# Optimization experiments

Hardware: AMD Instinct MI355X
Metric: run time of the kernel (lower is better)

The kernel has to match this reference:

```python
import jax, jax.numpy as jnp
from jax import lax
import numpy as np

B, C, H, W = 1, 128, 32, 32
OC, K = 128, 3
STRIDE, PAD, DIL = 1, 1, 1
ARRAY_SIZE = 32
QUANT = 8


def setup_inputs() -> dict:
    key = jax.random.key(0)
    k1, k2, k3 = jax.random.split(key, 3)
    x = jax.random.normal(k1, (B, C, H, W), dtype=jnp.float32)
    weight = jax.random.normal(k2, (OC, C, K, K), dtype=jnp.float32) * 0.05
    bias = jax.random.normal(k3, (OC,), dtype=jnp.float32) * 0.05
    return {"x": x, "weight": weight, "bias": bias}


def _conv(x, w, b):
    out = lax.conv_general_dilated(
        x, w, window_strides=(STRIDE, STRIDE),
        padding=((PAD, PAD), (PAD, PAD)),
        rhs_dilation=(DIL, DIL),
        dimension_numbers=("NCHW", "OIHW", "NCHW"))
    return out + b[None, :, None, None]


def _unfold(x, oh, ow):
    # torch F.unfold: (B, C*K*K, L) with channel-major ordering (c, kh, kw)
    xp = jnp.pad(x, ((0, 0), (0, 0), (PAD, PAD), (PAD, PAD)))
    cols = jnp.stack(
        [xp[:, :, i:i + oh, j:j + ow] for i in range(K) for j in range(K)],
        axis=2)  # (B, C, K*K, OH, OW)
    return cols.reshape(B, C * K * K, oh * ow)


def reference(x, weight, bias):
    oh = (H + 2 * PAD - DIL * (K - 1) - 1) // STRIDE + 1
    ow = (W + 2 * PAD - DIL * (K - 1) - 1) // STRIDE + 1
    L = oh * ow
    qmax = float(2 ** QUANT - 1)

    # --- set_quant_params: per-spatial-location scale/zero_point from full conv out ---
    out_full = _conv(x, weight, bias).reshape(1, OC, -1)  # (1, OC, L)
    mx = jnp.max(out_full, axis=1)  # (1, L)
    mn = jnp.min(out_full, axis=1)
    scale = (mx - mn) / qmax
    zp = jnp.clip(-mn / scale, 0.0, qmax)
    zp = jnp.where(jnp.isnan(zp), 0.0, zp)
    zp = jnp.trunc(zp)  # .int() truncation
    scale = lax.stop_gradient(scale)[:, None, None, :]  # (1,1,1,L)
    zp = lax.stop_gradient(zp)[:, None, None, :]

    # --- unfold + explicit elementwise multiply (crossbar expansion) ---
    cols = _unfold(x, oh, ow)                       # (B, C*K*K, L)
    pre = cols[:, None, :, :] * weight.reshape(1, OC, C * K * K, 1)  # (B,OC,CKK,L)

    # pad front of dim 2 to a multiple of array_size (pads a full chunk if divisible)
    ckk = C * K * K
    pad_d3 = ARRAY_SIZE - ckk % ARRAY_SIZE
    pre = jnp.pad(pre, ((0, 0), (0, 0), (pad_d3, 0), (0, 0)))

    # block-sum over array_size chunks (crossbar partial sums)
    n_chunks = (ckk + pad_d3) // ARRAY_SIZE
    accu = pre.reshape(B, OC, n_chunks, ARRAY_SIZE, L).sum(axis=3)  # (B,OC,n_chunks,L)

    # per-chunk fake-quant (Quant8F) with straight-through estimator
    q = jnp.clip(jnp.round(accu / scale) + zp, 0.0, qmax)
    deq = (q - zp) * scale
    quant_accu = accu + lax.stop_gradient(deq - accu)

    # reduce over chunks -> conv output (note: bias is NOT added in original forward)
    return quant_accu.sum(axis=2).reshape(B, OC, oh, ow)
```

## Files before the change

kernel.cpp:

```cpp
#include <hip/hip_runtime.h>

#define L_    1024
#define CKK_  1152
#define QMAX_ 255.0f
#define NCH   36

__global__ __launch_bounds__(256) void wtrans(
    const float* __restrict__ w, float* __restrict__ wt)
{
    const int e  = blockIdx.x * 256 + threadIdx.x;
    const int oc = e / 288, tq = e - 288 * oc;
    const float4 v = ((const float4*)(w + oc * CKK_))[tq];
    ((float4*)wt)[tq * 128 + oc] = v;
}

template <bool WT>
__global__ __launch_bounds__(512) void fused_cas(
    const float* __restrict__ x,
    const float* __restrict__ w,
    const float4* __restrict__ wt4,
    const float* __restrict__ bias,
    float* __restrict__ out)
{
    __shared__ __align__(16) float  xs[NCH * 32 * 4];
    __shared__ __align__(16) float4 vbuf[NCH][128];
    __shared__ float red[8][4];
    __shared__ float spar[2][2][3];
    __shared__ float qb[4][128];

    const int t   = threadIdx.x;
    const int b   = blockIdx.x;
    const int oc  = t & 127;
    const int g   = t >> 7;
    const int ppe = g & 1;
    const int oh  = b >> 3;
    const int ow0 = (b & 7) * 4;
    const int l0  = b * 4;
    const int jb  = g * 9;

    const float4* wrow = (const float4*)(w + oc * CKK_);

    auto load8 = [&](float4* dst, int j) {
#pragma unroll
        for (int k4 = 0; k4 < 8; ++k4)
            dst[k4] = WT ? wt4[(j * 8 + k4) * 128 + oc] : wrow[j * 8 + k4];
    };

    float4 wA[8], wB[8], wC[8];
    load8(wA, jb + 0);
    load8(wB, jb + 1);

    for (int i = 0; i < 9; ++i) {
        const int e   = i * 512 + t;
        const int j   = e >> 7;
        const int tap = (e >> 2) & 31;
        const int px  = e & 3;
        const int d   = j * 32 + tap;
        const int c   = d / 9, r = d - 9 * c;
        const int kh  = r / 3, kw = r - 3 * kh;
        const int iy  = oh + kh - 1, ix = ow0 + px + kw - 1;
        const bool ok = ((unsigned)iy < 32u) & ((unsigned)ix < 32u);
        const float vv = x[ok ? (c * 1024 + iy * 32 + ix) : 0];
        xs[e] = ok ? vv : 0.f;
    }
    __syncthreads();

    auto chunk = [&](int j, const float4* wreg) {
        float a0 = 0.f, a1 = 0.f, a2 = 0.f, a3 = 0.f;
        const float4* xj = (const float4*)(xs + j * 128);
#pragma unroll
        for (int k4 = 0; k4 < 8; ++k4) {
            const float4 wv = wreg[k4];
            const float4 x0 = xj[4 * k4 + 0];
            const float4 x1 = xj[4 * k4 + 1];
            const float4 x2 = xj[4 * k4 + 2];
            const float4 x3 = xj[4 * k4 + 3];
            a0 = fmaf(wv.x, x0.x, a0); a1 = fmaf(wv.x, x0.y, a1);
            a2 = fmaf(wv.x, x0.z, a2); a3 = fmaf(wv.x, x0.w, a3);
            a0 = fmaf(wv.y, x1.x, a0); a1 = fmaf(wv.y, x1.y, a1);
            a2 = fmaf(wv.y, x1.z, a2); a3 = fmaf(wv.y, x1.w, a3);
            a0 = fmaf(wv.z, x2.x, a0); a1 = fmaf(wv.z, x2.y, a1);
            a2 = fmaf(wv.z, x2.z, a2); a3 = fmaf(wv.z, x2.w, a3);
            a0 = fmaf(wv.w, x3.x, a0); a1 = fmaf(wv.w, x3.y, a1);
            a2 = fmaf(wv.w, x3.z, a2); a3 = fmaf(wv.w, x3.w, a3);
        }
        vbuf[j][oc] = make_float4(a0, a1, a2, a3);
    };

    load8(wC, jb + 2); chunk(jb + 0, wA);
    load8(wA, jb + 3); chunk(jb + 1, wB);
    load8(wB, jb + 4); chunk(jb + 2, wC);
    load8(wC, jb + 5); chunk(jb + 3, wA);
    load8(wA, jb + 6); chunk(jb + 4, wB);
    load8(wB, jb + 7); chunk(jb + 5, wC);
    load8(wC, jb + 8); chunk(jb + 6, wA);
    chunk(jb + 7, wB);
    chunk(jb + 8, wC);
    __syncthreads();

    float t0 = 0.f, t1 = 0.f;
    float mn0 = 0.f, mx0 = 0.f, mn1 = 0.f, mx1 = 0.f;
    const int wv = t >> 6;
    if (t < 256) {
        float s0 = 0.f, s1 = 0.f;
        for (int j = 0; j < NCH; ++j) {
            const float4 vv = vbuf[j][oc];
            s0 += (ppe == 0) ? vv.x : vv.z;
            s1 += (ppe == 0) ? vv.y : vv.w;
        }
        const float bval = bias[oc];
        t0 = s0 + bval; t1 = s1 + bval;

        mn0 = t0; mx0 = t0; mn1 = t1; mx1 = t1;
#pragma unroll
        for (int off = 32; off > 0; off >>= 1) {
            mn0 = fminf(mn0, __shfl_xor(mn0, off));
            mx0 = fmaxf(mx0, __shfl_xor(mx0, off));
            mn1 = fminf(mn1, __shfl_xor(mn1, off));
            mx1 = fmaxf(mx1, __shfl_xor(mx1, off));
        }
        if ((t & 63) == 0) {
            red[wv][0] = mn0; red[wv][1] = mx0;
            red[wv][2] = mn1; red[wv][3] = mx1;
        }
    }
    __syncthreads();
    if ((t & 63) == 0 && (wv & 1) == 0 && wv < 4) {
        const int pw = wv ^ 1;
        const float amn0 = fminf(mn0, red[pw][0]);
        const float amx0 = fmaxf(mx0, red[pw][1]);
        const float amn1 = fminf(mn1, red[pw][2]);
        const float amx1 = fmaxf(mx1, red[pw][3]);
        {
            const float sv = (amx0 - amn0) / QMAX_;
            float z = -amn0 / sv;
            z = fmaxf(z, 0.f);
            z = fminf(z, QMAX_);
            z = truncf(z);
            spar[ppe][0][0] = sv; spar[ppe][0][1] = z; spar[ppe][0][2] = 1.0f / sv;
        }
        {
            const float sv = (amx1 - amn1) / QMAX_;
            float z = -amn1 / sv;
            z = fmaxf(z, 0.f);
            z = fminf(z, QMAX_);
            z = truncf(z);
            spar[ppe][1][0] = sv; spar[ppe][1][1] = z; spar[ppe][1][2] = 1.0f / sv;
        }
    }
    __syncthreads();

    if (t < 256) {
        const float sc0 = spar[ppe][0][0], zp0 = spar[ppe][0][1], iv0 = spar[ppe][0][2];
        const float sc1 = spar[ppe][1][0], zp1 = spar[ppe][1][1], iv1 = spar[ppe][1][2];
        float q0 = 0.f, q1 = 0.f;
        for (int j = 0; j < NCH; ++j) {
            const float4 vv = vbuf[j][oc];
            const float v0 = (ppe == 0) ? vv.x : vv.z;
            const float v1 = (ppe == 0) ? vv.y : vv.w;
            float qn0 = rintf(v0 * iv0) + zp0;
            qn0 = fminf(fmaxf(qn0, 0.f), QMAX_);
            q0 += (qn0 - zp0) * sc0;
            float qn1 = rintf(v1 * iv1) + zp1;
            qn1 = fminf(fmaxf(qn1, 0.f), QMAX_);
            q1 += (qn1 - zp1) * sc1;
        }
        qb[2 * ppe + 0][oc] = q0;
        qb[2 * ppe + 1][oc] = q1;
    }
    __syncthreads();

    if (t < 128)
        *(float4*)(out + (size_t)t * L_ + l0) =
            make_float4(qb[0][t], qb[1][t], qb[2][t], qb[3][t]);
}

extern "C" void kernel_launch(void* const* d_in, const int* in_sizes, int n_in,
                              void* d_out, int out_size, void* d_ws, size_t ws_size,
                              hipStream_t stream) {
    const float* x    = (const float*)d_in[0];
    const float* w    = (const float*)d_in[1];
    const float* bias = (const float*)d_in[2];
    float* out = (float*)d_out;
    float* ws  = (float*)d_ws;

    const size_t wt_need = (size_t)288 * 128 * 16;
    if (ws_size >= wt_need) {
        wtrans<<<144, 256, 0, stream>>>(w, ws);
        fused_cas<true><<<256, 512, 0, stream>>>(
            x, w, (const float4*)ws, bias, out);
    } else {
        fused_cas<false><<<256, 512, 0, stream>>>(
            x, w, nullptr, bias, out);
    }
}
```

Measured before the change: 70.32 us.

## Keep chunk partial sums in registers and quantize per thread group

Each thread now keeps its nine chunk partial sums in registers instead of writing all 36 chunks to a large shared buffer. Group sums are combined through a small shared array, and the fake-quantisation runs in parallel across all 512 threads rather than 256 threads each looping over 36 chunks. Weight prefetching drops from triple to double buffering. The aim is to cut shared memory traffic and footprint and to spread the quantisation work, at the cost of more live registers and a change in summation order.

Result: faster. 67.74 us (-3.7%).

```diff
diff --git a/kernel.cpp b/kernel.cpp
--- a/kernel.cpp
+++ b/kernel.cpp
@@ -4,6 +4,10 @@
 #define CKK_  1152
 #define QMAX_ 255.0f
 #define NCH   36
+
+static __device__ __forceinline__ float4 f4add(float4 a, float4 b) {
+    return make_float4(a.x + b.x, a.y + b.y, a.z + b.z, a.w + b.w);
+}
 
 __global__ __launch_bounds__(256) void wtrans(
     const float* __restrict__ w, float* __restrict__ wt)
@@ -23,10 +27,9 @@
     float* __restrict__ out)
 {
     __shared__ __align__(16) float  xs[NCH * 32 * 4];
-    __shared__ __align__(16) float4 vbuf[NCH][128];
+    __shared__ __align__(16) float4 gx[4][128];
     __shared__ float red[8][4];
-    __shared__ float spar[2][2][3];
-    __shared__ float qb[4][128];
+    __shared__ float spar4[4][3];
 
     const int t   = threadIdx.x;
     const int b   = blockIdx.x;
@@ -46,7 +49,7 @@
             dst[k4] = WT ? wt4[(j * 8 + k4) * 128 + oc] : wrow[j * 8 + k4];
     };
 
-    float4 wA[8], wB[8], wC[8];
+    float4 wA[8], wB[8];
     load8(wA, jb + 0);
     load8(wB, jb + 1);
 
@@ -65,7 +68,7 @@
     }
     __syncthreads();
 
-    auto chunk = [&](int j, const float4* wreg) {
+    auto chunk = [&](int j, const float4* wreg) -> float4 {
         float a0 = 0.f, a1 = 0.f, a2 = 0.f, a3 = 0.f;
         const float4* xj = (const float4*)(xs + j * 128);
 #pragma unroll
@@ -84,32 +87,38 @@
             a0 = fmaf(wv.w, x3.x, a0); a1 = fmaf(wv.w, x3.y, a1);
             a2 = fmaf(wv.w, x3.z, a2); a3 = fmaf(wv.w, x3.w, a3);
         }
-        vbuf[j][oc] = make_float4(a0, a1, a2, a3);
+        return make_float4(a0, a1, a2, a3);
     };
 
-    load8(wC, jb + 2); chunk(jb + 0, wA);
-    load8(wA, jb + 3); chunk(jb + 1, wB);
-    load8(wB, jb + 4); chunk(jb + 2, wC);
-    load8(wC, jb + 5); chunk(jb + 3, wA);
-    load8(wA, jb + 6); chunk(jb + 4, wB);
-    load8(wB, jb + 7); chunk(jb + 5, wC);
-    load8(wC, jb + 8); chunk(jb + 6, wA);
-    chunk(jb + 7, wB);
-    chunk(jb + 8, wC);
+    float4 p0, p1, p2, p3, p4, p5, p6, p7, p8;
+    p0 = chunk(jb + 0, wA); load8(wA, jb + 2);
+    p1 = chunk(jb + 1, wB); load8(wB, jb + 3);
+    p2 = chunk(jb + 2, wA); load8(wA, jb + 4);
+    p3 = chunk(jb + 3, wB); load8(wB, jb + 5);
+    p4 = chunk(jb + 4, wA); load8(wA, jb + 6);
+    p5 = chunk(jb + 5, wB); load8(wB, jb + 7);
+    p6 = chunk(jb + 6, wA); load8(wA, jb + 8);
+    p7 = chunk(jb + 7, wB);
+    p8 = chunk(jb + 8, wA);
+
+    float4 gs = p0;
+    gs = f4add(gs, p1); gs = f4add(gs, p2); gs = f4add(gs, p3);
+    gs = f4add(gs, p4); gs = f4add(gs, p5); gs = f4add(gs, p6);
+    gs = f4add(gs, p7); gs = f4add(gs, p8);
+    gx[g][oc] = gs;
     __syncthreads();
 
     float t0 = 0.f, t1 = 0.f;
     float mn0 = 0.f, mx0 = 0.f, mn1 = 0.f, mx1 = 0.f;
     const int wv = t >> 6;
     if (t < 256) {
-        float s0 = 0.f, s1 = 0.f;
-        for (int j = 0; j < NCH; ++j) {
-            const float4 vv = vbuf[j][oc];
-            s0 += (ppe == 0) ? vv.x : vv.z;
-            s1 += (ppe == 0) ? vv.y : vv.w;
-        }
+        float4 s = gx[0][oc];
+        s = f4add(s, gx[1][oc]);
+        s = f4add(s, gx[2][oc]);
+        s = f4add(s, gx[3][oc]);
         const float bval = bias[oc];
-        t0 = s0 + bval; t1 = s1 + bval;
+        t0 = ((ppe == 0) ? s.x : s.z) + bval;
+        t1 = ((ppe == 0) ? s.y : s.w) + bval;
 
         mn0 = t0; mx0 = t0; mn1 = t1; mx1 = t1;
 #pragma unroll
@@ -137,7 +146,8 @@
             z = fmaxf(z, 0.f);
             z = fminf(z, QMAX_);
             z = truncf(z);
-            spar[ppe][0][0] = sv; spar[ppe][0][1] = z; spar[ppe][0][2] = 1.0f / sv;
+            spar4[2 * ppe + 0][0] = sv; spar4[2 * ppe + 0][1] = z;
+            spar4[2 * ppe + 0][2] = 1.0f / sv;
         }
         {
             const float sv = (amx1 - amn1) / QMAX_;
@@ -145,34 +155,40 @@
             z = fmaxf(z, 0.f);
             z = fminf(z, QMAX_);
             z = truncf(z);
-            spar[ppe][1][0] = sv; spar[ppe][1][1] = z; spar[ppe][1][2] = 1.0f / sv;
-        }
-    }
-    __syncthreads();
-
-    if (t < 256) {
-        const float sc0 = spar[ppe][0][0], zp0 = spar[ppe][0][1], iv0 = spar[ppe][0][2];
-        const float sc1 = spar[ppe][1][0], zp1 = spar[ppe][1][1], iv1 = spar[ppe][1][2];
-        float q0 = 0.f, q1 = 0.f;
-        for (int j = 0; j < NCH; ++j) {
-            const float4 vv = vbuf[j][oc];
-            const float v0 = (ppe == 0) ? vv.x : vv.z;
-            const float v1 = (ppe == 0) ? vv.y : vv.w;
-            float qn0 = rintf(v0 * iv0) + zp0;
-            qn0 = fminf(fmaxf(qn0, 0.f), QMAX_);
-            q0 += (qn0 - zp0) * sc0;
-            float qn1 = rintf(v1 * iv1) + zp1;
-            qn1 = fminf(fmaxf(qn1, 0.f), QMAX_);
-            q1 += (qn1 - zp1) * sc1;
-        }
-        qb[2 * ppe + 0][oc] = q0;
-        qb[2 * ppe + 1][oc] = q1;
-    }
-    __syncthreads();
-
-    if (t < 128)
-        *(float4*)(out + (size_t)t * L_ + l0) =
-            make_float4(qb[0][t], qb[1][t], qb[2][t], qb[3][t]);
+            spar4[2 * ppe + 1][0] = sv; spar4[2 * ppe + 1][1] = z;
+            spar4[2 * ppe + 1][2] = 1.0f / sv;
+        }
+    }
+    __syncthreads();
+
+    {
+        const float scx = spar4[0][0], zpx = spar4[0][1], ivx = spar4[0][2];
+        const float scy = spar4[1][0], zpy = spar4[1][1], ivy = spar4[1][2];
+        const float scz = spar4[2][0], zpz = spar4[2][1], ivz = spar4[2][2];
+        const float scw = spar4[3][0], zpw = spar4[3][1], ivw = spar4[3][2];
+
+        float qx = 0.f, qy = 0.f, qz = 0.f, qw = 0.f;
+        auto qstep = [&](const float4 p) {
+            float n;
+            n = rintf(p.x * ivx) + zpx; n = fminf(fmaxf(n, 0.f), QMAX_); qx += (n - zpx) * scx;
+            n = rintf(p.y * ivy) + zpy; n = fminf(fmaxf(n, 0.f), QMAX_); qy += (n - zpy) * scy;
+            n = rintf(p.z * ivz) + zpz; n = fminf(fmaxf(n, 0.f), QMAX_); qz += (n - zpz) * scz;
+            n = rintf(p.w * ivw) + zpw; n = fminf(fmaxf(n, 0.f), QMAX_); qw += (n - zpw) * scw;
+        };
+        qstep(p0); qstep(p1); qstep(p2); qstep(p3); qstep(p4);
+        qstep(p5); qstep(p6); qstep(p7); qstep(p8);
+
+        gx[g][oc] = make_float4(qx, qy, qz, qw);
+    }
+    __syncthreads();
+
+    if (t < 128) {
+        float4 f = gx[0][t];
+        f = f4add(f, gx[1][t]);
+        f = f4add(f, gx[2][t]);
+        f = f4add(f, gx[3][t]);
+        *(float4*)(out + (size_t)t * L_ + l0) = f;
+    }
 }
 
 extern "C" void kernel_launch(void* const* d_in, const int* in_sizes, int n_in,
```
